# Kernel optimization log

Measured on AMD Instinct MI355X. Metric: run time of the kernel, lower is better.

## Reference

```python
import jax, jax.numpy as jnp
import numpy as np

T, B = 2048, 128
H = 128          # hidden_size
QH = 1024        # query_hidden_size
NF = 32          # num_convolution_filters
K = 31           # convolution_filter_size (odd, same padding)


def setup_inputs() -> dict:
    key = jax.random.key(0)
    ks = jax.random.split(key, 10)
    encoded_tokens = jax.random.normal(ks[0], (T, B, H), dtype=jnp.float32)
    tokens_mask = jax.random.randint(ks[1], (B, T), 0, 2).astype(jnp.bool_)
    query = jax.random.normal(ks[2], (1, B, QH), dtype=jnp.float32)
    cumulative_alignment = jax.random.uniform(ks[3], (B, T), dtype=jnp.float32)
    # parameters
    conv_w = jax.random.normal(ks[4], (NF, 1, K), dtype=jnp.float32) * 0.1   # Conv1d weight [out,in,k]
    conv_b = jnp.zeros((NF,), dtype=jnp.float32)
    Wq = jax.random.normal(ks[5], (H, QH), dtype=jnp.float32) * (1.0 / np.sqrt(QH))
    bq = jnp.zeros((H,), dtype=jnp.float32)
    Wa = jax.random.normal(ks[6], (H, NF), dtype=jnp.float32) * (1.0 / np.sqrt(NF))
    ba = jnp.zeros((H,), dtype=jnp.float32)
    score_w = jax.random.normal(ks[7], (H,), dtype=jnp.float32) * (1.0 / np.sqrt(H))  # xavier-ish
    score_b = jnp.zeros((H,), dtype=jnp.float32)
    return dict(encoded_tokens=encoded_tokens, tokens_mask=tokens_mask, query=query,
                cumulative_alignment=cumulative_alignment, conv_w=conv_w, conv_b=conv_b,
                Wq=Wq, bq=bq, Wa=Wa, ba=ba, score_w=score_w, score_b=score_b)


def reference(encoded_tokens, tokens_mask, query, cumulative_alignment,
              conv_w, conv_b, Wq, bq, Wa, ba, score_w, score_b):
    # location features: Conv1d over cumulative alignment, same padding
    loc = jax.lax.conv_general_dilated(
        cumulative_alignment[:, None, :], conv_w,
        window_strides=(1,), padding=[((K - 1) // 2, (K - 1) // 2)],
        dimension_numbers=('NCH', 'OIH', 'NCH'))  # [B, NF, T]
    loc = loc + conv_b[None, :, None]
    loc = jnp.transpose(loc, (2, 0, 1))                        # [T, B, NF]
    loc = jnp.einsum('tbf,hf->tbh', loc, Wa) + ba              # [T, B, H]
    q = jnp.einsum('obq,hq->obh', query, Wq) + bq              # [1, B, H]
    # additive score: tanh of fused elementwise sum, then project to scalar
    score = jnp.tanh(encoded_tokens + q + loc + score_b)       # [T, B, H]
    s = jnp.einsum('tbh,h->bt', score, score_w)                # [B, T]
    s = jnp.where(tokens_mask, -jnp.inf, s)
    alignment = jax.nn.softmax(s, axis=1)                      # [B, T]
    context = jnp.einsum('bt,tbh->bh', alignment, encoded_tokens)  # [B, H]
    cumulative_alignment = cumulative_alignment + alignment
    return context, cumulative_alignment, alignment
```

## Files before the change

### kernel.cpp

```cpp
#include <hip/hip_runtime.h>
#include <stdint.h>

#define T_DIM 2048
#define B_DIM 128
#define H_DIM 128
#define QH_DIM 1024
#define NF 32
#define KW 31
#define TB 128
#define NTILE (T_DIM / TB)
#define CPAD_ROW (T_DIM + 32)

#define NEG_INF (-__builtin_inff())

typedef float v2f __attribute__((ext_vector_type(2)));

__device__ __forceinline__ float fast_tanh(float x) {
    float e = __expf(2.0f * x);
    return 1.0f - 2.0f * __builtin_amdgcn_rcpf(1.0f + e);
}

template <int C>
__device__ __forceinline__ float dpp_add(float x) {
    int m = __builtin_amdgcn_update_dpp(0, __float_as_int(x), C, 0xf, 0xf, true);
    return x + __int_as_float(m);
}
__device__ __forceinline__ float wave_sum64(float x) {
    x = dpp_add<0x111>(x); x = dpp_add<0x112>(x); x = dpp_add<0x114>(x); x = dpp_add<0x118>(x);
    x = dpp_add<0x142>(x); x = dpp_add<0x143>(x);
    return __int_as_float(__builtin_amdgcn_readlane(__float_as_int(x), 63));
}

__global__ __launch_bounds__(256)
void k_prep(const float* __restrict__ cum, const void* __restrict__ mask,
            float* __restrict__ cpad, float* __restrict__ mbias) {
    const int gid = blockIdx.x * 256 + threadIdx.x;
    const int b = gid >> 11, t = gid & 2047;
    const int l = threadIdx.x & 63;
    uint32_t u = ((const uint32_t*)mask)[l];
    unsigned long long hi = __ballot(u > 1u);
    unsigned long long nf = __ballot(u != 0u && u != 0x3f800000u);
    int layout = (hi == 0ull) ? 0 : ((nf == 0ull) ? 2 : 1);
    bool m;
    if (layout == 0)      m = ((const int32_t*)mask)[gid] != 0;
    else if (layout == 1) m = ((const uint8_t*)mask)[gid] != 0;
    else                  m = ((const float*)mask)[gid] != 0.0f;
    mbias[gid] = m ? NEG_INF : 0.0f;
    cpad[b * CPAD_ROW + 16 + t] = cum[gid];
    if (t < 16) cpad[b * CPAD_ROW + t] = 0.0f;
    else if (t >= T_DIM - 16) cpad[b * CPAD_ROW + 32 + t] = 0.0f;
}

__global__ void k0_G(const float* __restrict__ Wa, const float* __restrict__ conv_w,
                     float* __restrict__ Gt) {
    int gid = blockIdx.x * blockDim.x + threadIdx.x;
    if (gid >= KW * H_DIM) return;
    int k = gid >> 7, h = gid & 127;
    float acc = 0.0f;
    #pragma unroll
    for (int f = 0; f < NF; ++f) acc = fmaf(Wa[h * NF + f], conv_w[f * KW + k], acc);
    Gt[gid] = acc;
}

__global__ __launch_bounds__(512)
void k1_query(const float* __restrict__ query, const float* __restrict__ Wq,
              const float* __restrict__ bq, const float* __restrict__ Wa,
              const float* __restrict__ conv_b, const float* __restrict__ ba,
              const float* __restrict__ score_b, float* __restrict__ qb) {
    const int b = blockIdx.x, tid = threadIdx.x;
    const int h = tid & 127, qtr = tid >> 7;
    __shared__ __align__(16) float qrow[QH_DIM];
    __shared__ float partial[512];
    for (int i = tid; i < QH_DIM; i += 512) qrow[i] = query[b * QH_DIM + i];
    __syncthreads();
    const float4* wq4 = (const float4*)(Wq + (size_t)h * QH_DIM + qtr * 256);
    const float4* q4 = (const float4*)(qrow + qtr * 256);
    float acc = 0.0f;
    #pragma unroll 4
    for (int j = 0; j < 64; ++j) {
        float4 w = wq4[j], q = q4[j];
        acc += w.x * q.x + w.y * q.y + w.z * q.z + w.w * q.w;
    }
    if (qtr == 0) {
        float cb = bq[h] + ba[h] + score_b[h];
        #pragma unroll
        for (int f = 0; f < NF; ++f) cb = fmaf(Wa[h * NF + f], conv_b[f], cb);
        acc += cb;
    }
    partial[tid] = acc;
    __syncthreads();
    if (tid < 128) qb[b * H_DIM + h] = partial[h] + partial[h + 128] + partial[h + 256] + partial[h + 384];
}

__global__ __launch_bounds__(256, 2)
void k2_fused(const float* __restrict__ enc, const float* __restrict__ cpad,
              const float* __restrict__ mbias, const float* __restrict__ Gt,
              const float* __restrict__ qb, const float* __restrict__ score_w,
              float* __restrict__ s_out, float* __restrict__ o_part,
              float* __restrict__ ml_part) {
    const int b = blockIdx.x;
    const int tl = blockIdx.y;
    const int tid = threadIdx.x;
    const int l = tid & 63;
    const int wv = __builtin_amdgcn_readfirstlane(tid >> 6);
    const int tw0 = tl * TB + wv * 32;

    __shared__ float oc[4][H_DIM];
    __shared__ float mwl[4], lwl[4];

    v2f G[KW];
    #pragma unroll
    for (int k = 0; k < KW; ++k) G[k] = *(const v2f*)(Gt + k * H_DIM + 2 * l);

    const v2f base = *(const v2f*)(qb + b * H_DIM + 2 * l);
    const v2f w2 = *(const v2f*)(score_w + 2 * l);
    const float* crow = cpad + b * CPAD_ROW;
    const float* mrow = mbias + b * T_DIM;

    float m_w = NEG_INF, l_w = 0.0f;
    v2f o = {0.0f, 0.0f};
    float sv = 0.0f;

    #pragma unroll
    for (int c = 0; c < 4; ++c) {
        const int tb = tw0 + c * 8;

        float sc[38];
        #pragma unroll
        for (int j = 0; j < 38; ++j) sc[j] = crow[tb + 1 + j];

        v2f ee[8];
        #pragma unroll
        for (int it = 0; it < 8; ++it)
            ee[it] = *(const v2f*)(enc + ((size_t)(tb + it) * B_DIM + b) * H_DIM + 2 * l);

        float su[8];
        #pragma unroll
        for (int it = 0; it < 8; ++it) {
            v2f acc = base;
            #pragma unroll
            for (int k = 0; k < KW; ++k)
                acc = __builtin_elementwise_fma(G[k], (v2f){sc[it + k], sc[it + k]}, acc);
            const v2f a2 = acc + ee[it];
            float p = w2.x * fast_tanh(a2.x) + w2.y * fast_tanh(a2.y);
            su[it] = wave_sum64(p) + mrow[tb + it];
        }

        #pragma unroll
        for (int it = 0; it < 8; ++it) sv = (l == c * 8 + it) ? su[it] : sv;

        float m8 = su[0];
        #pragma unroll
        for (int it = 1; it < 8; ++it) m8 = fmaxf(m8, su[it]);
        const float m_new = fmaxf(m_w, m8);
        const float m_use = (m_new == NEG_INF) ? 0.0f : m_new;
        const float alpha = __expf(m_w - m_use);
        float lsum = 0.0f;
        v2f osum = {0.0f, 0.0f};
        #pragma unroll
        for (int it = 0; it < 8; ++it) {
            const float e = __expf(su[it] - m_use);
            lsum += e;
            osum = __builtin_elementwise_fma((v2f){e, e}, ee[it], osum);
        }
        l_w = fmaf(l_w, alpha, lsum);
        o = __builtin_elementwise_fma(o, (v2f){alpha, alpha}, osum);
        m_w = m_new;
    }

    if (l < 32) s_out[b * T_DIM + tw0 + l] = sv;

    oc[wv][2 * l] = o.x;
    oc[wv][2 * l + 1] = o.y;
    if (l == 0) { mwl[wv] = m_w; lwl[wv] = l_w; }
    __syncthreads();
    if (tid < H_DIM) {
        const float mb = fmaxf(fmaxf(mwl[0], mwl[1]), fmaxf(mwl[2], mwl[3]));
        const float mu = (mb == NEG_INF) ? 0.0f : mb;
        const float b0 = __expf(mwl[0] - mu), b1 = __expf(mwl[1] - mu);
        const float b2 = __expf(mwl[2] - mu), b3 = __expf(mwl[3] - mu);
        const float ov = oc[0][tid] * b0 + oc[1][tid] * b1 + oc[2][tid] * b2 + oc[3][tid] * b3;
        const int tbase = b * NTILE + tl;
        o_part[tbase * H_DIM + tid] = ov;
        if (tid == 0) {
            ml_part[tbase * 2] = mb;
            ml_part[tbase * 2 + 1] = lwl[0] * b0 + lwl[1] * b1 + lwl[2] * b2 + lwl[3] * b3;
        }
    }
}

__global__ __launch_bounds__(256)
void k5_final(float* __restrict__ s_align, const float* __restrict__ cum_in,
              float* __restrict__ cum_out, const float* __restrict__ o_part,
              const float* __restrict__ ml_part, float* __restrict__ ctx) {
    const int b = blockIdx.x, tid = threadIdx.x;
    __shared__ float sm[NTILE], sl[NTILE], sb[NTILE];
    if (tid < NTILE) {
        sm[tid] = ml_part[(b * NTILE + tid) * 2];
        sl[tid] = ml_part[(b * NTILE + tid) * 2 + 1];
    }
    __syncthreads();
    float M = sm[0];
    #pragma unroll
    for (int i = 1; i < NTILE; ++i) M = fmaxf(M, sm[i]);
    const float M_use = (M == NEG_INF) ? 0.0f : M;
    if (tid < NTILE) sb[tid] = __expf(sm[tid] - M_use);
    __syncthreads();
    float L = 0.0f;
    #pragma unroll
    for (int i = 0; i < NTILE; ++i) L = fmaf(sl[i], sb[i], L);
    const float invL = 1.0f / L;
    if (tid < H_DIM) {
        float ov = 0.0f;
        #pragma unroll
        for (int i = 0; i < NTILE; ++i)
            ov = fmaf(o_part[(b * NTILE + i) * H_DIM + tid], sb[i], ov);
        ctx[b * H_DIM + tid] = ov * invL;
    }
    #pragma unroll
    for (int j = 0; j < 8; ++j) {
        const int idx = b * T_DIM + tid + j * 256;
        const float a = __expf(s_align[idx] - M_use) * invL;
        s_align[idx] = a;
        cum_out[idx] = cum_in[idx] + a;
    }
}

extern "C" void kernel_launch(void* const* d_in, const int* in_sizes, int n_in,
                              void* d_out, int out_size, void* d_ws, size_t ws_size,
                              hipStream_t stream) {
    const float* enc     = (const float*)d_in[0];
    const void*  mask    = d_in[1];
    const float* query   = (const float*)d_in[2];
    const float* cum     = (const float*)d_in[3];
    const float* conv_w  = (const float*)d_in[4];
    const float* conv_b  = (const float*)d_in[5];
    const float* Wq      = (const float*)d_in[6];
    const float* bq      = (const float*)d_in[7];
    const float* Wa      = (const float*)d_in[8];
    const float* ba      = (const float*)d_in[9];
    const float* score_w = (const float*)d_in[10];
    const float* score_b = (const float*)d_in[11];

    float* ctx_out   = (float*)d_out;
    float* cum_out   = ctx_out + B_DIM * H_DIM;
    float* align_out = cum_out + B_DIM * T_DIM;

    float* Gt     = (float*)d_ws;
    float* qb     = Gt + 4096;
    float* o_part = qb + B_DIM * H_DIM;
    float* ml     = o_part + B_DIM * NTILE * H_DIM;
    float* cpad   = ml + 8192;
    float* mb     = cpad + B_DIM * CPAD_ROW;

    k_prep<<<B_DIM * T_DIM / 256, 256, 0, stream>>>(cum, mask, cpad, mb);
    k0_G<<<16, 256, 0, stream>>>(Wa, conv_w, Gt);
    k1_query<<<B_DIM, 512, 0, stream>>>(query, Wq, bq, Wa, conv_b, ba, score_b, qb);
    k2_fused<<<dim3(B_DIM, NTILE), 256, 0, stream>>>(enc, cpad, mb, Gt, qb, score_w,
                                                     align_out, o_part, ml);
    k5_final<<<B_DIM, 256, 0, stream>>>(align_out, cum, cum_out, o_part, ml, ctx_out);
}
```

Baseline: 244.6 us.

## Merge setup kernels into one launch and fold final reduction into main kernel

Combines the prep, G-matrix and query-projection kernels into a single kernel that dispatches on block index. The separate final softmax/context kernel is removed: each tile block increments a per-batch atomic counter, and the last block to arrive does the cross-tile reduction, normalisation and cumulative update. This cuts launch count from five to two and removes launch gaps, at the cost of threadfences, an atomic per block, and a serialized tail on the last-arriving block for each batch row.

Result: slower. 519.3 us (+112.3%).

```diff
diff --git a/kernel.cpp b/kernel.cpp
--- a/kernel.cpp
+++ b/kernel.cpp
@@ -32,72 +32,76 @@
 }
 
 __global__ __launch_bounds__(256)
-void k_prep(const float* __restrict__ cum, const void* __restrict__ mask,
-            float* __restrict__ cpad, float* __restrict__ mbias) {
-    const int gid = blockIdx.x * 256 + threadIdx.x;
-    const int b = gid >> 11, t = gid & 2047;
-    const int l = threadIdx.x & 63;
-    uint32_t u = ((const uint32_t*)mask)[l];
-    unsigned long long hi = __ballot(u > 1u);
-    unsigned long long nf = __ballot(u != 0u && u != 0x3f800000u);
-    int layout = (hi == 0ull) ? 0 : ((nf == 0ull) ? 2 : 1);
-    bool m;
-    if (layout == 0)      m = ((const int32_t*)mask)[gid] != 0;
-    else if (layout == 1) m = ((const uint8_t*)mask)[gid] != 0;
-    else                  m = ((const float*)mask)[gid] != 0.0f;
-    mbias[gid] = m ? NEG_INF : 0.0f;
-    cpad[b * CPAD_ROW + 16 + t] = cum[gid];
-    if (t < 16) cpad[b * CPAD_ROW + t] = 0.0f;
-    else if (t >= T_DIM - 16) cpad[b * CPAD_ROW + 32 + t] = 0.0f;
-}
-
-__global__ void k0_G(const float* __restrict__ Wa, const float* __restrict__ conv_w,
-                     float* __restrict__ Gt) {
-    int gid = blockIdx.x * blockDim.x + threadIdx.x;
-    if (gid >= KW * H_DIM) return;
-    int k = gid >> 7, h = gid & 127;
-    float acc = 0.0f;
-    #pragma unroll
-    for (int f = 0; f < NF; ++f) acc = fmaf(Wa[h * NF + f], conv_w[f * KW + k], acc);
-    Gt[gid] = acc;
-}
-
-__global__ __launch_bounds__(512)
-void k1_query(const float* __restrict__ query, const float* __restrict__ Wq,
-              const float* __restrict__ bq, const float* __restrict__ Wa,
-              const float* __restrict__ conv_b, const float* __restrict__ ba,
-              const float* __restrict__ score_b, float* __restrict__ qb) {
-    const int b = blockIdx.x, tid = threadIdx.x;
-    const int h = tid & 127, qtr = tid >> 7;
+void k_setup(const float* __restrict__ cum, const void* __restrict__ mask,
+             const float* __restrict__ query, const float* __restrict__ Wq,
+             const float* __restrict__ bq, const float* __restrict__ Wa,
+             const float* __restrict__ conv_b, const float* __restrict__ ba,
+             const float* __restrict__ score_b, const float* __restrict__ conv_w,
+             float* __restrict__ cpad, float* __restrict__ mbias,
+             float* __restrict__ Gt, float* __restrict__ qb, int* __restrict__ cnt) {
+    const int bid = blockIdx.x, tid = threadIdx.x;
     __shared__ __align__(16) float qrow[QH_DIM];
-    __shared__ float partial[512];
-    for (int i = tid; i < QH_DIM; i += 512) qrow[i] = query[b * QH_DIM + i];
-    __syncthreads();
-    const float4* wq4 = (const float4*)(Wq + (size_t)h * QH_DIM + qtr * 256);
-    const float4* q4 = (const float4*)(qrow + qtr * 256);
-    float acc = 0.0f;
-    #pragma unroll 4
-    for (int j = 0; j < 64; ++j) {
-        float4 w = wq4[j], q = q4[j];
-        acc += w.x * q.x + w.y * q.y + w.z * q.z + w.w * q.w;
-    }
-    if (qtr == 0) {
-        float cb = bq[h] + ba[h] + score_b[h];
-        #pragma unroll
-        for (int f = 0; f < NF; ++f) cb = fmaf(Wa[h * NF + f], conv_b[f], cb);
-        acc += cb;
-    }
-    partial[tid] = acc;
-    __syncthreads();
-    if (tid < 128) qb[b * H_DIM + h] = partial[h] + partial[h + 128] + partial[h + 256] + partial[h + 384];
+    __shared__ float partial[256];
+
+    if (bid < 1024) {
+        const int gid = bid * 256 + tid;
+        const int b = gid >> 11, t = gid & 2047;
+        const int l = tid & 63;
+        uint32_t u = ((const uint32_t*)mask)[l];
+        unsigned long long hi = __ballot(u > 1u);
+        unsigned long long nf = __ballot(u != 0u && u != 0x3f800000u);
+        int layout = (hi == 0ull) ? 0 : ((nf == 0ull) ? 2 : 1);
+        bool m;
+        if (layout == 0)      m = ((const int32_t*)mask)[gid] != 0;
+        else if (layout == 1) m = ((const uint8_t*)mask)[gid] != 0;
+        else                  m = ((const float*)mask)[gid] != 0.0f;
+        mbias[gid] = m ? NEG_INF : 0.0f;
+        cpad[b * CPAD_ROW + 16 + t] = cum[gid];
+        if (t < 16) cpad[b * CPAD_ROW + t] = 0.0f;
+        else if (t >= T_DIM - 16) cpad[b * CPAD_ROW + 32 + t] = 0.0f;
+        if (gid < B_DIM) cnt[gid] = 0;
+    } else if (bid < 1040) {
+        const int gid = (bid - 1024) * 256 + tid;
+        if (gid < KW * H_DIM) {
+            const int k = gid >> 7, h = gid & 127;
+            float acc = 0.0f;
+            #pragma unroll
+            for (int f = 0; f < NF; ++f) acc = fmaf(Wa[h * NF + f], conv_w[f * KW + k], acc);
+            Gt[gid] = acc;
+        }
+    } else {
+        const int b = bid - 1040;
+        for (int i = tid; i < QH_DIM; i += 256) qrow[i] = query[b * QH_DIM + i];
+        __syncthreads();
+        const int h = tid & 127, half = tid >> 7;
+        const float4* wq4 = (const float4*)(Wq + (size_t)h * QH_DIM + half * 512);
+        const float4* q4 = (const float4*)(qrow + half * 512);
+        float acc = 0.0f;
+        #pragma unroll 4
+        for (int j = 0; j < 128; ++j) {
+            float4 w = wq4[j], q = q4[j];
+            acc += w.x * q.x + w.y * q.y + w.z * q.z + w.w * q.w;
+        }
+        if (half == 0) {
+            float cb = bq[h] + ba[h] + score_b[h];
+            #pragma unroll
+            for (int f = 0; f < NF; ++f) cb = fmaf(Wa[h * NF + f], conv_b[f], cb);
+            acc += cb;
+        }
+        partial[tid] = acc;
+        __syncthreads();
+        if (tid < 128) qb[b * H_DIM + h] = partial[h] + partial[h + 128];
+    }
 }
 
 __global__ __launch_bounds__(256, 2)
 void k2_fused(const float* __restrict__ enc, const float* __restrict__ cpad,
               const float* __restrict__ mbias, const float* __restrict__ Gt,
               const float* __restrict__ qb, const float* __restrict__ score_w,
+              const float* __restrict__ cum_in,
               float* __restrict__ s_out, float* __restrict__ o_part,
-              float* __restrict__ ml_part) {
+              float* __restrict__ ml_part, float* __restrict__ ctx,
+              float* __restrict__ cum_out, int* __restrict__ cnt) {
     const int b = blockIdx.x;
     const int tl = blockIdx.y;
     const int tid = threadIdx.x;
@@ -107,6 +111,8 @@
 
     __shared__ float oc[4][H_DIM];
     __shared__ float mwl[4], lwl[4];
+    __shared__ int is_last;
+    __shared__ float sm[NTILE], sl[NTILE], sbv[NTILE];
 
     v2f G[KW];
     #pragma unroll
@@ -187,14 +193,14 @@
             ml_part[tbase * 2 + 1] = lwl[0] * b0 + lwl[1] * b1 + lwl[2] * b2 + lwl[3] * b3;
         }
     }
-}
-
-__global__ __launch_bounds__(256)
-void k5_final(float* __restrict__ s_align, const float* __restrict__ cum_in,
-              float* __restrict__ cum_out, const float* __restrict__ o_part,
-              const float* __restrict__ ml_part, float* __restrict__ ctx) {
-    const int b = blockIdx.x, tid = threadIdx.x;
-    __shared__ float sm[NTILE], sl[NTILE], sb[NTILE];
+
+    __threadfence();
+    __syncthreads();
+    if (tid == 0) is_last = (atomicAdd(&cnt[b], 1) == NTILE - 1) ? 1 : 0;
+    __syncthreads();
+    if (!is_last) return;
+
+    __threadfence();
     if (tid < NTILE) {
         sm[tid] = ml_part[(b * NTILE + tid) * 2];
         sl[tid] = ml_part[(b * NTILE + tid) * 2 + 1];
@@ -204,24 +210,24 @@
     #pragma unroll
     for (int i = 1; i < NTILE; ++i) M = fmaxf(M, sm[i]);
     const float M_use = (M == NEG_INF) ? 0.0f : M;
-    if (tid < NTILE) sb[tid] = __expf(sm[tid] - M_use);
+    if (tid < NTILE) sbv[tid] = __expf(sm[tid] - M_use);
     __syncthreads();
     float L = 0.0f;
     #pragma unroll
-    for (int i = 0; i < NTILE; ++i) L = fmaf(sl[i], sb[i], L);
+    for (int i = 0; i < NTILE; ++i) L = fmaf(sl[i], sbv[i], L);
     const float invL = 1.0f / L;
     if (tid < H_DIM) {
         float ov = 0.0f;
         #pragma unroll
         for (int i = 0; i < NTILE; ++i)
-            ov = fmaf(o_part[(b * NTILE + i) * H_DIM + tid], sb[i], ov);
+            ov = fmaf(o_part[(b * NTILE + i) * H_DIM + tid], sbv[i], ov);
         ctx[b * H_DIM + tid] = ov * invL;
     }
     #pragma unroll
     for (int j = 0; j < 8; ++j) {
         const int idx = b * T_DIM + tid + j * 256;
-        const float a = __expf(s_align[idx] - M_use) * invL;
-        s_align[idx] = a;
+        const float a = __expf(s_out[idx] - M_use) * invL;
+        s_out[idx] = a;
         cum_out[idx] = cum_in[idx] + a;
     }
 }
@@ -252,11 +258,11 @@
     float* ml     = o_part + B_DIM * NTILE * H_DIM;
     float* cpad   = ml + 8192;
     float* mb     = cpad + B_DIM * CPAD_ROW;
-
-    k_prep<<<B_DIM * T_DIM / 256, 256, 0, stream>>>(cum, mask, cpad, mb);
-    k0_G<<<16, 256, 0, stream>>>(Wa, conv_w, Gt);
-    k1_query<<<B_DIM, 512, 0, stream>>>(query, Wq, bq, Wa, conv_b, ba, score_b, qb);
+    int*   cnt    = (int*)(mb + B_DIM * T_DIM);
+
+    k_setup<<<1168, 256, 0, stream>>>(cum, mask, query, Wq, bq, Wa, conv_b, ba,
+                                      score_b, conv_w, cpad, mb, Gt, qb, cnt);
     k2_fused<<<dim3(B_DIM, NTILE), 256, 0, stream>>>(enc, cpad, mb, Gt, qb, score_w,
-                                                     align_out, o_part, ml);
-    k5_final<<<B_DIM, 256, 0, stream>>>(align_out, cum, cum_out, o_part, ml, ctx_out);
-}
+                                                     cum, align_out, o_part, ml,
+                                                     ctx_out, cum_out, cnt);
+}
```
